# Kernel optimization log

Hardware: AMD Instinct MI355X
Metric: run time of the kernel (lower is better)

## Reference

```python
import jax, jax.numpy as jnp
import numpy as np

N_NODES = 50000

def _sage_conv(x, src, dst, W_l, b_l, W_r):
    # mean-aggregate neighbor features: messages x[src] summed into dst
    msgs = x[src]                                   # [E, d]
    agg = jax.ops.segment_sum(msgs, dst, num_segments=N_NODES)  # [N, d]
    ones = jnp.ones((src.shape[0],), dtype=x.dtype)
    cnt = jax.ops.segment_sum(ones, dst, num_segments=N_NODES)  # [N]
    agg = agg / jnp.maximum(cnt, 1.0)[:, None]
    return agg @ W_l + b_l + x @ W_r


def setup_inputs() -> dict:
    key = jax.random.key(0)
    ks = jax.random.split(key, 8)
    d_in, hid, out = 64, 128, 64
    x = jax.random.normal(ks[0], (N_NODES, d_in), dtype=jnp.float32)
    edge_index = jax.random.randint(ks[1], (2, 1600000), 0, N_NODES, dtype=jnp.int64)
    def w(k, a, b):
        return jax.random.normal(k, (a, b), dtype=jnp.float32) / np.sqrt(a)
    return {
        "x": x,
        "edge_index": edge_index,
        "W_l1": w(ks[2], d_in, hid), "b_l1": jnp.zeros((hid,), jnp.float32),
        "W_r1": w(ks[3], d_in, hid),
        "W_l2": w(ks[4], hid, hid), "b_l2": jnp.zeros((hid,), jnp.float32),
        "W_r2": w(ks[5], hid, hid),
        "W_out": w(ks[6], hid, out), "b_out": jnp.zeros((out,), jnp.float32),
    }


def reference(x, edge_index, W_l1, b_l1, W_r1, W_l2, b_l2, W_r2, W_out, b_out):
    src, dst = edge_index[0], edge_index[1]
    h = jax.nn.relu(_sage_conv(x, src, dst, W_l1, b_l1, W_r1))
    h = jax.nn.relu(_sage_conv(h, src, dst, W_l2, b_l2, W_r2))
    return h @ W_out + b_out
```

## Files before the change

### kernel.cpp

```cpp
#include <hip/hip_runtime.h>


typedef unsigned short ushort_t;
typedef unsigned int uint_t;
typedef unsigned char uchar_t;
typedef __attribute__((ext_vector_type(8))) short short8;
typedef __attribute__((ext_vector_type(8))) ushort_t ushort8;
typedef __attribute__((ext_vector_type(4))) float f32x4;

#define BKT_SHIFT 7
#define BKT_NODES 128
#define BKT_CAP   5120
#define EPB       4096
#define QSCALE    32.0f
#define QINV      0.03125f

__device__ inline ushort_t bf16_rne(float v) {
    uint_t u = __float_as_uint(v);
    u += 0x7fffu + ((u >> 16) & 1u);
    return (ushort_t)(u >> 16);
}
__device__ inline float bf16_to_f(ushort_t h) {
    return __uint_as_float((uint_t)h << 16);
}


struct WPack {
    const float* srcp[5];
    ushort_t* dstp[5];
    int K[5], N[5], beg[5], end[5];
};

__global__ __launch_bounds__(1024)
void k_work(const int* __restrict__ src, const int* __restrict__ dst,
            uint_t* __restrict__ pairs, int* __restrict__ bcnt, int E, int nbk,
            int bbl, const float* __restrict__ x, ushort_t* __restrict__ xh,
            ushort_t* __restrict__ xl, int NS, WPack wp, int total) {
    int tid = threadIdx.x;
    if (blockIdx.x >= bbl) {
        int t = (blockIdx.x - bbl) * 1024 + tid;
        if (t < NS) {
            float v = x[t];
            ushort_t h = bf16_rne(v);
            xh[t] = h;
            xl[t] = bf16_rne(v - bf16_to_f(h));
            return;
        }
        t -= NS;
        if (t >= total) return;
#pragma unroll
        for (int m = 0; m < 5; ++m) {
            if (t >= wp.beg[m] && t < wp.end[m]) {
                int i = t - wp.beg[m];
                int K = wp.K[m], N = wp.N[m];
                int k = i / N, nn = i % N;
                int NT = N >> 4;
                int kt = k >> 5, bq = (k >> 3) & 3, j = k & 7;
                int nt = nn >> 4, lane = (bq << 4) | (nn & 15);
                int base = (((kt * NT + nt) << 6) + lane) * 8 + j;
                int halfsz = (K >> 5) * NT * 512;
                float v = wp.srcp[m][i];
                ushort_t h = bf16_rne(v);
                wp.dstp[m][base] = h;
                wp.dstp[m][halfsz + base] = bf16_rne(v - bf16_to_f(h));
            }
        }
        return;
    }

    __shared__ int h[4][512];
    int sub = tid & 3;
    for (int i = tid; i < 4 * 512; i += 1024) ((int*)h)[i] = 0;
    __syncthreads();

    int e = blockIdx.x * EPB + tid * 4;
    bool full = (e + 4 <= E);
    int4 d4 = {0, 0, 0, 0}, s4 = {0, 0, 0, 0};
    if (full) {
        d4 = *(const int4*)(dst + e);
        s4 = *(const int4*)(src + e);
        atomicAdd(&h[sub][d4.x >> BKT_SHIFT], 1);
        atomicAdd(&h[sub][d4.y >> BKT_SHIFT], 1);
        atomicAdd(&h[sub][d4.z >> BKT_SHIFT], 1);
        atomicAdd(&h[sub][d4.w >> BKT_SHIFT], 1);
    } else {
        for (int t = e; t < E && t < e + 4; ++t)
            atomicAdd(&h[sub][dst[t] >> BKT_SHIFT], 1);
    }
    __syncthreads();
    for (int i = tid; i < nbk; i += 1024) {
        int c0 = h[0][i], c1 = h[1][i], c2 = h[2][i], c3 = h[3][i];
        int c = c0 + c1 + c2 + c3;
        int bs = c ? atomicAdd(&bcnt[i], c) : 0;
        h[0][i] = bs; h[1][i] = bs + c0; h[2][i] = bs + c0 + c1;
        h[3][i] = bs + c0 + c1 + c2;
    }
    __syncthreads();
    if (full) {
        int dd[4] = {d4.x, d4.y, d4.z, d4.w};
        int ss[4] = {s4.x, s4.y, s4.z, s4.w};
#pragma unroll
        for (int t = 0; t < 4; ++t) {
            int b = dd[t] >> BKT_SHIFT;
            int r = atomicAdd(&h[sub][b], 1);
            pairs[(size_t)b * BKT_CAP + r] =
                (uint_t)(ss[t] & 0xFFFF) | ((uint_t)(dd[t] & (BKT_NODES - 1)) << 16);
        }
    } else {
        for (int t = e; t < E && t < e + 4; ++t) {
            int d = dst[t];
            int b = d >> BKT_SHIFT;
            int r = atomicAdd(&h[sub][b], 1);
            pairs[(size_t)b * BKT_CAP + r] =
                (uint_t)(src[t] & 0xFFFF) | ((uint_t)(d & (BKT_NODES - 1)) << 16);
        }
    }
}


__global__ __launch_bounds__(1024) void k_csr(const uint_t* __restrict__ pairs,
                                              const int* __restrict__ bcnt,
                                              int* __restrict__ off,
                                              ushort_t* __restrict__ col, int n) {
    __shared__ int hist[BKT_NODES];
    __shared__ int s[BKT_NODES];
    __shared__ int cur[BKT_NODES];
    __shared__ int bofs_s;
    int b = blockIdx.x, tid = threadIdx.x;
    if (tid < 64) {
        int p = 0;
        for (int i = tid; i < b; i += 64) p += bcnt[i];
#pragma unroll
        for (int m = 1; m < 64; m <<= 1) p += __shfl_xor(p, m);
        if (tid == 0) bofs_s = p;
    }
    if (tid < BKT_NODES) hist[tid] = 0;
    __syncthreads();
    int bofs = bofs_s;
    int cnt = bcnt[b];
    const uint_t* p = pairs + (size_t)b * BKT_CAP;
    for (int i = tid; i < cnt; i += 1024) atomicAdd(&hist[(p[i] >> 16) & 127], 1);
    __syncthreads();
    int v = (tid < BKT_NODES) ? hist[tid] : 0;
    if (tid < BKT_NODES) s[tid] = v;
    __syncthreads();
    for (int ofs = 1; ofs < BKT_NODES; ofs <<= 1) {
        int t = (tid >= ofs && tid < BKT_NODES) ? s[tid - ofs] : 0;
        __syncthreads();
        if (tid < BKT_NODES) s[tid] += t;
        __syncthreads();
    }
    if (tid < BKT_NODES) {
        int excl = bofs + s[tid] - v;
        int node = b * BKT_NODES + tid;
        if (node <= n) off[node] = excl;
        cur[tid] = excl;
    }
    __syncthreads();
    for (int i = tid; i < cnt; i += 1024) {
        uint_t pk = p[i];
        int pos = atomicAdd(&cur[(pk >> 16) & 127], 1);
        col[pos] = (ushort_t)(pk & 0xFFFF);
    }
}


__device__ inline void accum2(float2 (&a)[4], uint4 q) {
    const uint_t* u = (const uint_t*)&q;
#pragma unroll
    for (int i = 0; i < 4; ++i) {
        a[i].x += __uint_as_float(u[i] << 16);
        a[i].y += __uint_as_float(u[i] & 0xffff0000u);
    }
}
__device__ inline void accum2m(float2 (&a)[4], uint4 q, float m) {
    const uint_t* u = (const uint_t*)&q;
#pragma unroll
    for (int i = 0; i < 4; ++i) {
        a[i].x = fmaf(m, __uint_as_float(u[i] << 16), a[i].x);
        a[i].y = fmaf(m, __uint_as_float(u[i] & 0xffff0000u), a[i].y);
    }
}

template <int DIN>
__device__ inline void agg_node(const ushort_t* __restrict__ fbase,
                                const ushort_t* __restrict__ col,
                                int s0, int s1, int sub, float2 (&a2)[4]) {
    constexpr int LPR = DIN / 8, EPI = 64 / LPR;
    constexpr int DEEP = (DIN == 128) ? 8 : 4;
#pragma unroll
    for (int j = 0; j < 4; ++j) a2[j] = (float2){0.f, 0.f};
    int e = s0;
    for (; e + DEEP * EPI <= s1; e += DEEP * EPI) {
        int c[DEEP];
        uint4 q[DEEP];
#pragma unroll
        for (int j = 0; j < DEEP; ++j) c[j] = col[e + j * EPI + sub];
#pragma unroll
        for (int j = 0; j < DEEP; ++j) q[j] = *(const uint4*)(fbase + (size_t)c[j] * DIN);
#pragma unroll
        for (int j = 0; j < DEEP; ++j) accum2(a2, q[j]);
    }
    for (; e < s1; e += 4 * EPI) {
        int last = s1 - 1;
        int i0 = e + sub, i1 = i0 + EPI, i2 = i1 + EPI, i3 = i2 + EPI;
        float m0 = (i0 < s1) ? 1.f : 0.f;
        float m1 = (i1 < s1) ? 1.f : 0.f;
        float m2 = (i2 < s1) ? 1.f : 0.f;
        float m3 = (i3 < s1) ? 1.f : 0.f;
        int c0 = col[min(i0, last)];
        int c1 = col[min(i1, last)];
        int c2 = col[min(i2, last)];
        int c3 = col[min(i3, last)];
        uint4 q0 = *(const uint4*)(fbase + (size_t)c0 * DIN);
        uint4 q1 = *(const uint4*)(fbase + (size_t)c1 * DIN);
        uint4 q2 = *(const uint4*)(fbase + (size_t)c2 * DIN);
        uint4 q3 = *(const uint4*)(fbase + (size_t)c3 * DIN);
        accum2m(a2, q0, m0); accum2m(a2, q1, m1);
        accum2m(a2, q2, m2); accum2m(a2, q3, m3);
    }
}

__global__ __launch_bounds__(256)
void k_agg_u8(const uchar_t* __restrict__ fq, const int* __restrict__ off,
              const ushort_t* __restrict__ col,
              ushort_t* __restrict__ ah, ushort_t* __restrict__ al, int n) {
    constexpr int EPI = 8;
    int wave = (int)((blockIdx.x * (unsigned)blockDim.x + threadIdx.x) >> 6);
    int lane = threadIdx.x & 63;
    if (wave >= n) return;
    int li = lane & 7;
    int sub = lane >> 3;
    int s0 = off[wave], s1 = off[wave + 1];
    const uchar_t* fbase = fq + li * 16;

    uint_t ae[4] = {0, 0, 0, 0}, ao[4] = {0, 0, 0, 0};
    int e = s0;
    for (; e + 4 * EPI <= s1; e += 4 * EPI) {
        int c[4];
        uint4 q[4];
#pragma unroll
        for (int j = 0; j < 4; ++j) c[j] = col[e + j * EPI + sub];
#pragma unroll
        for (int j = 0; j < 4; ++j) q[j] = *(const uint4*)(fbase + (size_t)c[j] * 128);
#pragma unroll
        for (int j = 0; j < 4; ++j) {
            const uint_t* u = (const uint_t*)&q[j];
#pragma unroll
            for (int i = 0; i < 4; ++i) {
                ae[i] += u[i] & 0x00FF00FFu;
                ao[i] += (u[i] >> 8) & 0x00FF00FFu;
            }
        }
    }
    if (e < s1) {
        int last = s1 - 1;
        int idx[4];
        uint_t msk[4];
        int c[4];
        uint4 q[4];
#pragma unroll
        for (int j = 0; j < 4; ++j) {
            idx[j] = e + j * EPI + sub;
            msk[j] = (idx[j] < s1) ? 0xFFFFFFFFu : 0u;
            c[j] = col[min(idx[j], last)];
        }
#pragma unroll
        for (int j = 0; j < 4; ++j) q[j] = *(const uint4*)(fbase + (size_t)c[j] * 128);
#pragma unroll
        for (int j = 0; j < 4; ++j) {
            const uint_t* u = (const uint_t*)&q[j];
#pragma unroll
            for (int i = 0; i < 4; ++i) {
                uint_t um = u[i] & msk[j];
                ae[i] += um & 0x00FF00FFu;
                ao[i] += (um >> 8) & 0x00FF00FFu;
            }
        }
    }
#pragma unroll
    for (int m = 8; m < 64; m <<= 1) {
#pragma unroll
        for (int i = 0; i < 4; ++i) {
            ae[i] += __shfl_xor(ae[i], m);
            ao[i] += __shfl_xor(ao[i], m);
        }
    }
    if (sub == 0) {
        float inv = QINV / fmaxf((float)(s1 - s0), 1.f);
        ushort_t vh[16], vl[16];
#pragma unroll
        for (int i = 0; i < 4; ++i) {
            uint_t f[4] = {ae[i] & 0xFFFFu, ao[i] & 0xFFFFu,
                           ae[i] >> 16, ao[i] >> 16};
#pragma unroll
            for (int b = 0; b < 4; ++b) {
                float mval = (float)f[b] * inv;
                ushort_t h = bf16_rne(mval);
                vh[i * 4 + b] = h;
                vl[i * 4 + b] = bf16_rne(mval - bf16_to_f(h));
            }
        }
        size_t o = (size_t)wave * 128 + li * 16;
        *(ushort8*)(ah + o) = *(ushort8*)&vh[0];
        *(ushort8*)(ah + o + 8) = *(ushort8*)&vh[8];
        *(ushort8*)(al + o) = *(ushort8*)&vl[0];
        *(ushort8*)(al + o + 8) = *(ushort8*)&vl[8];
    }
}

__device__ inline f32x4 mfma3(f32x4 acc, short8 ah, short8 al, short8 bh, short8 bl) {
    acc = __builtin_amdgcn_mfma_f32_16x16x32_bf16(ah, bh, acc, 0, 0, 0);
    acc = __builtin_amdgcn_mfma_f32_16x16x32_bf16(al, bh, acc, 0, 0, 0);
    acc = __builtin_amdgcn_mfma_f32_16x16x32_bf16(ah, bl, acc, 0, 0, 0);
    return acc;
}

template <int DIN, int DOUT, int M2>
__device__ inline void mfma_pass(const ushort_t* __restrict__ Fh,
                                 const ushort_t* __restrict__ Fl,
                                 const ushort_t* __restrict__ Wp,
                                 f32x4 (&acc)[M2][DOUT / 16],
                                 int base, int n, int lane) {
    constexpr int KT = DIN / 32, NT = DOUT / 16;
    int col = lane & 15, quad = lane >> 4;
    short8 fh[M2][KT], fl[M2][KT];
#pragma unroll
    for (int c = 0; c < M2; ++c) {
        int row = base + c * 16 + col;
        if (row >= n) row = n - 1;
        size_t roff = (size_t)row * DIN + quad * 8;
#pragma unroll
        for (int kt = 0; kt < KT; ++kt) {
            fh[c][kt] = *(const short8*)(Fh + roff + kt * 32);
            fl[c][kt] = *(const short8*)(Fl + roff + kt * 32);
        }
    }
#pragma unroll
    for (int nt = 0; nt < NT; ++nt) {
#pragma unroll
        for (int kt = 0; kt < KT; ++kt) {
            const ushort_t* p = Wp + ((size_t)((kt * NT + nt) << 6) + lane) * 8;
            short8 bh = *(const short8*)p;
            short8 bl = *(const short8*)(p + (size_t)KT * NT * 512);
#pragma unroll
            for (int c = 0; c < M2; ++c)
                acc[c][nt] = mfma3(acc[c][nt], fh[c][kt], fl[c][kt], bh, bl);
        }
    }
}


__global__ __launch_bounds__(512)
void k_layer1(const ushort_t* __restrict__ xh, const ushort_t* __restrict__ xl,
              const int* __restrict__ off, const ushort_t* __restrict__ col,
              const ushort_t* __restrict__ Wlp, const ushort_t* __restrict__ Wrp,
              const float* __restrict__ bias, ushort_t* __restrict__ Oh,
              ushort_t* __restrict__ Ol, uchar_t* __restrict__ Oq, int n) {
    constexpr int LPR = 8;
    __shared__ ushort_t Ahs[32][72];
    __shared__ ushort_t Als[32][72];
    int tid = threadIdx.x, waveid = tid >> 6, lane = tid & 63;
    int base = blockIdx.x * 32;
    int li = lane & (LPR - 1);
    int sub = lane / LPR;

    for (int q = 0; q < 4; ++q) {
        int node = base + waveid * 4 + q;
        int nd = node < n ? node : n - 1;
        int s0 = off[nd], s1 = off[nd + 1];
        float2 a2[4];
        agg_node<64>(xh + li * 8, col, s0, s1, sub, a2);
#pragma unroll
        for (int m = LPR; m < 64; m <<= 1) {
#pragma unroll
            for (int j = 0; j < 4; ++j) {
                a2[j].x += __shfl_xor(a2[j].x, m);
                a2[j].y += __shfl_xor(a2[j].y, m);
            }
        }
        if (sub == 0) {
            float inv = 1.f / fmaxf((float)(s1 - s0), 1.f);
            ushort8 vh, vl;
#pragma unroll
            for (int j = 0; j < 4; ++j) {
                float mx = a2[j].x * inv, my = a2[j].y * inv;
                ushort_t hx = bf16_rne(mx), hy = bf16_rne(my);
                vh[2 * j] = hx;     vl[2 * j] = bf16_rne(mx - bf16_to_f(hx));
                vh[2 * j + 1] = hy; vl[2 * j + 1] = bf16_rne(my - bf16_to_f(hy));
            }
            *(ushort8*)&Ahs[waveid * 4 + q][li * 8] = vh;
            *(ushort8*)&Als[waveid * 4 + q][li * 8] = vl;
        }
    }
    __syncthreads();

    int rowt = waveid >> 2, c0 = waveid & 3;
    int colq = lane & 15, quad = lane >> 4;
    int arow = rowt * 16 + colq;
    short8 fah[2], fal[2], fxh[2], fxl[2];
#pragma unroll
    for (int kt = 0; kt < 2; ++kt) {
        fah[kt] = *(const short8*)&Ahs[arow][kt * 32 + quad * 8];
        fal[kt] = *(const short8*)&Als[arow][kt * 32 + quad * 8];
    }
    int grow = base + arow; if (grow >= n) grow = n - 1;
#pragma unroll
    for (int kt = 0; kt < 2; ++kt) {
        fxh[kt] = *(const short8*)(xh + (size_t)grow * 64 + kt * 32 + quad * 8);
        fxl[kt] = *(const short8*)(xl + (size_t)grow * 64 + kt * 32 + quad * 8);
    }
#pragma unroll
    for (int t = 0; t < 2; ++t) {
        int nt = c0 + t * 4;
        float bv = bias[nt * 16 + colq];
        f32x4 acc = (f32x4){bv, bv, bv, bv};
#pragma unroll
        for (int kt = 0; kt < 2; ++kt) {
            const ushort_t* pL = Wlp + ((size_t)((kt * 8 + nt) << 6) + lane) * 8;
            acc = mfma3(acc, fah[kt], fal[kt],
                        *(const short8*)pL, *(const short8*)(pL + 8192));
            const ushort_t* pR = Wrp + ((size_t)((kt * 8 + nt) << 6) + lane) * 8;
            acc = mfma3(acc, fxh[kt], fxl[kt],
                        *(const short8*)pR, *(const short8*)(pR + 8192));
        }
        int rowb = base + rowt * 16 + quad * 4;
        int cix = nt * 16 + colq;
#pragma unroll
        for (int r = 0; r < 4; ++r) {
            int row = rowb + r;
            if (row < n) {
                float v = fmaxf(acc[r], 0.f);
                ushort_t h = bf16_rne(v);
                Oh[(size_t)row * 128 + cix] = h;
                Ol[(size_t)row * 128 + cix] = bf16_rne(v - bf16_to_f(h));
                int qv = (int)(v * QSCALE + 0.5f);
                Oq[(size_t)row * 128 + cix] = (uchar_t)(qv > 255 ? 255 : qv);
            }
        }
    }
}


#define LROW 136
__global__ __launch_bounds__(256)
void k_dense23(const ushort_t* __restrict__ Ah, const ushort_t* __restrict__ Al,
               const ushort_t* __restrict__ Xh, const ushort_t* __restrict__ Xl,
               const ushort_t* __restrict__ Wlp, const ushort_t* __restrict__ Wrp,
               const float* __restrict__ b2, const ushort_t* __restrict__ Wop,
               const float* __restrict__ bo, float* __restrict__ out, int n) {
    constexpr int DIN = 128, DOUT = 128, NT = DOUT / 16;
    __shared__ ushort_t lds[4][2][16 * LROW];
    int waveid = threadIdx.x >> 6;
    int lane = threadIdx.x & 63;
    int wave = (blockIdx.x * blockDim.x + threadIdx.x) >> 6;
    int nw = (n + 15) / 16;
    if (wave >= nw) wave = nw - 1;
    int base = wave * 16;
    int col = lane & 15, quad = lane >> 4;

    f32x4 acc[1][NT];
#pragma unroll
    for (int nt = 0; nt < NT; ++nt) {
        float bv = b2[nt * 16 + col];
        acc[0][nt] = (f32x4){bv, bv, bv, bv};
    }
    mfma_pass<DIN, DOUT, 1>(Ah, Al, Wlp, acc, base, n, lane);
    mfma_pass<DIN, DOUT, 1>(Xh, Xl, Wrp, acc, base, n, lane);

    ushort_t* Lh = &lds[waveid][0][0];
    ushort_t* Ll = &lds[waveid][1][0];
#pragma unroll
    for (int nt = 0; nt < NT; ++nt) {
        int cix = nt * 16 + col;
#pragma unroll
        for (int r = 0; r < 4; ++r) {
            int row = quad * 4 + r;
            float v = fmaxf(acc[0][nt][r], 0.f);
            ushort_t h = bf16_rne(v);
            Lh[row * LROW + cix] = h;
            Ll[row * LROW + cix] = bf16_rne(v - bf16_to_f(h));
        }
    }
    __syncthreads();

    constexpr int KT2 = 4, NT2 = 4;
    short8 ah[KT2], al[KT2];
    int arow = lane & 15;
#pragma unroll
    for (int kt = 0; kt < KT2; ++kt) {
        ah[kt] = *(const short8*)(Lh + arow * LROW + kt * 32 + quad * 8);
        al[kt] = *(const short8*)(Ll + arow * LROW + kt * 32 + quad * 8);
    }
    f32x4 acc2[NT2];
#pragma unroll
    for (int nt = 0; nt < NT2; ++nt) {
        float bv = bo[nt * 16 + col];
        acc2[nt] = (f32x4){bv, bv, bv, bv};
    }
#pragma unroll
    for (int nt = 0; nt < NT2; ++nt) {
#pragma unroll
        for (int kt = 0; kt < KT2; ++kt) {
            const ushort_t* p = Wop + ((size_t)((kt * 4 + nt) << 6) + lane) * 8;
            acc2[nt] = mfma3(acc2[nt], ah[kt], al[kt],
                             *(const short8*)p, *(const short8*)(p + 8192));
        }
    }
    int rowb = base + quad * 4;
#pragma unroll
    for (int nt = 0; nt < NT2; ++nt) {
        int cix = nt * 16 + col;
#pragma unroll
        for (int r = 0; r < 4; ++r) {
            int row = rowb + r;
            if (row < n) out[(size_t)row * 64 + cix] = acc2[nt][r];
        }
    }
}


static inline size_t align256(size_t x) { return (x + 255) & ~(size_t)255; }

extern "C" void kernel_launch(void* const* d_in, const int* in_sizes, int n_in,
                              void* d_out, int out_size, void* d_ws, size_t ws_size,
                              hipStream_t stream) {
    const float* x   = (const float*)d_in[0];
    const int*   ei  = (const int*)d_in[1];
    const float* Wl1 = (const float*)d_in[2];
    const float* bl1 = (const float*)d_in[3];
    const float* Wr1 = (const float*)d_in[4];
    const float* Wl2 = (const float*)d_in[5];
    const float* bl2 = (const float*)d_in[6];
    const float* Wr2 = (const float*)d_in[7];
    const float* Wo  = (const float*)d_in[8];
    const float* bo  = (const float*)d_in[9];

    const int N = in_sizes[0] / 64;
    const int E = in_sizes[1] / 2;
    const int* src = ei;
    const int* dst = ei + E;
    const int nbk = (N + BKT_NODES - 1) >> BKT_SHIFT;

    char* ws = (char*)d_ws;
    int* off = (int*)ws;            ws += align256((size_t)(N + 1) * 4);
    int* bcnt = (int*)ws;           ws += align256((size_t)nbk * 4);
    uint_t* pairs = (uint_t*)ws;    ws += align256((size_t)nbk * BKT_CAP * 4);
    ushort_t* col = (ushort_t*)ws;  ws += align256((size_t)E * 2);
    ushort_t* xh  = (ushort_t*)ws;  ws += align256((size_t)N * 64 * 2);
    ushort_t* xl  = (ushort_t*)ws;  ws += align256((size_t)N * 64 * 2);
    ushort_t* h1h = (ushort_t*)ws;  ws += align256((size_t)N * 128 * 2);
    ushort_t* h1l = (ushort_t*)ws;  ws += align256((size_t)N * 128 * 2);
    uchar_t*  h1q = (uchar_t*)ws;   ws += align256((size_t)N * 128);
    ushort_t* a2h = (ushort_t*)ws;  ws += align256((size_t)N * 128 * 2);
    ushort_t* a2l = (ushort_t*)ws;  ws += align256((size_t)N * 128 * 2);
    ushort_t* Wl1p = (ushort_t*)ws; ws += align256((size_t)2 * 64 * 128 * 2);
    ushort_t* Wr1p = (ushort_t*)ws; ws += align256((size_t)2 * 64 * 128 * 2);
    ushort_t* Wl2p = (ushort_t*)ws; ws += align256((size_t)2 * 128 * 128 * 2);
    ushort_t* Wr2p = (ushort_t*)ws; ws += align256((size_t)2 * 128 * 128 * 2);
    ushort_t* Wop  = (ushort_t*)ws; ws += align256((size_t)2 * 128 * 64 * 2);

    WPack wp;
    wp.srcp[0] = Wl1; wp.dstp[0] = Wl1p; wp.K[0] = 64;  wp.N[0] = 128;
    wp.srcp[1] = Wr1; wp.dstp[1] = Wr1p; wp.K[1] = 64;  wp.N[1] = 128;
    wp.srcp[2] = Wl2; wp.dstp[2] = Wl2p; wp.K[2] = 128; wp.N[2] = 128;
    wp.srcp[3] = Wr2; wp.dstp[3] = Wr2p; wp.K[3] = 128; wp.N[3] = 128;
    wp.srcp[4] = Wo;  wp.dstp[4] = Wop;  wp.K[4] = 128; wp.N[4] = 64;
    int acc_el = 0;
    for (int m = 0; m < 5; ++m) {
        wp.beg[m] = acc_el; acc_el += wp.K[m] * wp.N[m]; wp.end[m] = acc_el;
    }
    int NS = N * 64;

    hipMemsetAsync(bcnt, 0, (size_t)nbk * 4, stream);
    int bbl = (E + EPB - 1) / EPB;
    int pbl = (NS + acc_el + 1023) / 1024;
    k_work<<<bbl + pbl, 1024, 0, stream>>>(src, dst, pairs, bcnt, E, nbk, bbl,
                                           x, xh, xl, NS, wp, acc_el);

    k_csr<<<nbk, 1024, 0, stream>>>(pairs, bcnt, off, col, N);

    k_layer1<<<(N + 31) / 32, 512, 0, stream>>>(xh, xl, off, col, Wl1p, Wr1p,
                                                bl1, h1h, h1l, h1q, N);

    int aggbl = (N * 64 + 255) / 256;
    k_agg_u8<<<aggbl, 256, 0, stream>>>(h1q, off, col, a2h, a2l, N);

    int dbl2 = ((N + 15) / 16 + 3) / 4;
    k_dense23<<<dbl2, 256, 0, stream>>>(a2h, a2l, h1h, h1l, Wl2p, Wr2p, bl2,
                                        Wop, bo, (float*)d_out, N);
}
```

Measured before the change: 231.6 us.

## Quantize layer-1 gather to uint8 and fuse layer-2 aggregation with dense stages

```diff
diff --git a/kernel.cpp b/kernel.cpp
--- a/kernel.cpp
+++ b/kernel.cpp
@@ -14,6 +14,7 @@
 #define EPB       4096
 #define QSCALE    32.0f
 #define QINV      0.03125f
+#define XQSCALE   16.0f
 
 __device__ inline ushort_t bf16_rne(float v) {
     uint_t u = __float_as_uint(v);
@@ -35,7 +36,8 @@
 void k_work(const int* __restrict__ src, const int* __restrict__ dst,
             uint_t* __restrict__ pairs, int* __restrict__ bcnt, int E, int nbk,
             int bbl, const float* __restrict__ x, ushort_t* __restrict__ xh,
-            ushort_t* __restrict__ xl, int NS, WPack wp, int total) {
+            ushort_t* __restrict__ xl, uchar_t* __restrict__ xq,
+            int NS, WPack wp, int total) {
     int tid = threadIdx.x;
     if (blockIdx.x >= bbl) {
         int t = (blockIdx.x - bbl) * 1024 + tid;
@@ -44,6 +46,9 @@
             ushort_t h = bf16_rne(v);
             xh[t] = h;
             xl[t] = bf16_rne(v - bf16_to_f(h));
+            int qv = (int)(v * XQSCALE + 128.5f);
+            qv = qv < 0 ? 0 : (qv > 255 ? 255 : qv);
+            xq[t] = (uchar_t)qv;
             return;
         }
         t -= NS;
@@ -164,77 +169,14 @@
     }
 }
 
-
-__device__ inline void accum2(float2 (&a)[4], uint4 q) {
-    const uint_t* u = (const uint_t*)&q;
-#pragma unroll
-    for (int i = 0; i < 4; ++i) {
-        a[i].x += __uint_as_float(u[i] << 16);
-        a[i].y += __uint_as_float(u[i] & 0xffff0000u);
-    }
-}
-__device__ inline void accum2m(float2 (&a)[4], uint4 q, float m) {
-    const uint_t* u = (const uint_t*)&q;
-#pragma unroll
-    for (int i = 0; i < 4; ++i) {
-        a[i].x = fmaf(m, __uint_as_float(u[i] << 16), a[i].x);
-        a[i].y = fmaf(m, __uint_as_float(u[i] & 0xffff0000u), a[i].y);
-    }
-}
-
-template <int DIN>
-__device__ inline void agg_node(const ushort_t* __restrict__ fbase,
-                                const ushort_t* __restrict__ col,
-                                int s0, int s1, int sub, float2 (&a2)[4]) {
-    constexpr int LPR = DIN / 8, EPI = 64 / LPR;
-    constexpr int DEEP = (DIN == 128) ? 8 : 4;
-#pragma unroll
-    for (int j = 0; j < 4; ++j) a2[j] = (float2){0.f, 0.f};
-    int e = s0;
-    for (; e + DEEP * EPI <= s1; e += DEEP * EPI) {
-        int c[DEEP];
-        uint4 q[DEEP];
-#pragma unroll
-        for (int j = 0; j < DEEP; ++j) c[j] = col[e + j * EPI + sub];
-#pragma unroll
-        for (int j = 0; j < DEEP; ++j) q[j] = *(const uint4*)(fbase + (size_t)c[j] * DIN);
-#pragma unroll
-        for (int j = 0; j < DEEP; ++j) accum2(a2, q[j]);
-    }
-    for (; e < s1; e += 4 * EPI) {
-        int last = s1 - 1;
-        int i0 = e + sub, i1 = i0 + EPI, i2 = i1 + EPI, i3 = i2 + EPI;
-        float m0 = (i0 < s1) ? 1.f : 0.f;
-        float m1 = (i1 < s1) ? 1.f : 0.f;
-        float m2 = (i2 < s1) ? 1.f : 0.f;
-        float m3 = (i3 < s1) ? 1.f : 0.f;
-        int c0 = col[min(i0, last)];
-        int c1 = col[min(i1, last)];
-        int c2 = col[min(i2, last)];
-        int c3 = col[min(i3, last)];
-        uint4 q0 = *(const uint4*)(fbase + (size_t)c0 * DIN);
-        uint4 q1 = *(const uint4*)(fbase + (size_t)c1 * DIN);
-        uint4 q2 = *(const uint4*)(fbase + (size_t)c2 * DIN);
-        uint4 q3 = *(const uint4*)(fbase + (size_t)c3 * DIN);
-        accum2m(a2, q0, m0); accum2m(a2, q1, m1);
-        accum2m(a2, q2, m2); accum2m(a2, q3, m3);
-    }
-}
-
-__global__ __launch_bounds__(256)
-void k_agg_u8(const uchar_t* __restrict__ fq, const int* __restrict__ off,
-              const ushort_t* __restrict__ col,
-              ushort_t* __restrict__ ah, ushort_t* __restrict__ al, int n) {
-    constexpr int EPI = 8;
-    int wave = (int)((blockIdx.x * (unsigned)blockDim.x + threadIdx.x) >> 6);
-    int lane = threadIdx.x & 63;
-    if (wave >= n) return;
-    int li = lane & 7;
-    int sub = lane >> 3;
-    int s0 = off[wave], s1 = off[wave + 1];
-    const uchar_t* fbase = fq + li * 16;
-
-    uint_t ae[4] = {0, 0, 0, 0}, ao[4] = {0, 0, 0, 0};
+template <int ROWB>
+__device__ inline void gather_u8(const uchar_t* __restrict__ fbase,
+                                 const ushort_t* __restrict__ col,
+                                 int s0, int s1, int sub,
+                                 uint_t (&ae)[4], uint_t (&ao)[4]) {
+    constexpr int EPI = 1024 / ROWB;
+#pragma unroll
+    for (int i = 0; i < 4; ++i) { ae[i] = 0u; ao[i] = 0u; }
     int e = s0;
     for (; e + 4 * EPI <= s1; e += 4 * EPI) {
         int c[4];
@@ -242,7 +184,7 @@
 #pragma unroll
         for (int j = 0; j < 4; ++j) c[j] = col[e + j * EPI + sub];
 #pragma unroll
-        for (int j = 0; j < 4; ++j) q[j] = *(const uint4*)(fbase + (size_t)c[j] * 128);
+        for (int j = 0; j < 4; ++j) q[j] = *(const uint4*)(fbase + (size_t)c[j] * ROWB);
 #pragma unroll
         for (int j = 0; j < 4; ++j) {
             const uint_t* u = (const uint_t*)&q[j];
@@ -253,22 +195,21 @@
             }
         }
     }
-    if (e < s1) {
+    for (; e < s1; e += 2 * EPI) {
         int last = s1 - 1;
-        int idx[4];
-        uint_t msk[4];
-        int c[4];
-        uint4 q[4];
-#pragma unroll
-        for (int j = 0; j < 4; ++j) {
-            idx[j] = e + j * EPI + sub;
-            msk[j] = (idx[j] < s1) ? 0xFFFFFFFFu : 0u;
-            c[j] = col[min(idx[j], last)];
-        }
-#pragma unroll
-        for (int j = 0; j < 4; ++j) q[j] = *(const uint4*)(fbase + (size_t)c[j] * 128);
-#pragma unroll
-        for (int j = 0; j < 4; ++j) {
+        int c[2];
+        uint_t msk[2];
+        uint4 q[2];
+#pragma unroll
+        for (int j = 0; j < 2; ++j) {
+            int idx = e + j * EPI + sub;
+            msk[j] = (idx < s1) ? 0xFFFFFFFFu : 0u;
+            c[j] = col[min(idx, last)];
+        }
+#pragma unroll
+        for (int j = 0; j < 2; ++j) q[j] = *(const uint4*)(fbase + (size_t)c[j] * ROWB);
+#pragma unroll
+        for (int j = 0; j < 2; ++j) {
             const uint_t* u = (const uint_t*)&q[j];
 #pragma unroll
             for (int i = 0; i < 4; ++i) {
@@ -277,35 +218,6 @@
                 ao[i] += (um >> 8) & 0x00FF00FFu;
             }
         }
-    }
-#pragma unroll
-    for (int m = 8; m < 64; m <<= 1) {
-#pragma unroll
-        for (int i = 0; i < 4; ++i) {
-            ae[i] += __shfl_xor(ae[i], m);
-            ao[i] += __shfl_xor(ao[i], m);
-        }
-    }
-    if (sub == 0) {
-        float inv = QINV / fmaxf((float)(s1 - s0), 1.f);
-        ushort_t vh[16], vl[16];
-#pragma unroll
-        for (int i = 0; i < 4; ++i) {
-            uint_t f[4] = {ae[i] & 0xFFFFu, ao[i] & 0xFFFFu,
-                           ae[i] >> 16, ao[i] >> 16};
-#pragma unroll
-            for (int b = 0; b < 4; ++b) {
-                float mval = (float)f[b] * inv;
-                ushort_t h = bf16_rne(mval);
-                vh[i * 4 + b] = h;
-                vl[i * 4 + b] = bf16_rne(mval - bf16_to_f(h));
-            }
-        }
-        size_t o = (size_t)wave * 128 + li * 16;
-        *(ushort8*)(ah + o) = *(ushort8*)&vh[0];
-        *(ushort8*)(ah + o + 8) = *(ushort8*)&vh[8];
-        *(ushort8*)(al + o) = *(ushort8*)&vl[0];
-        *(ushort8*)(al + o + 8) = *(ushort8*)&vl[8];
     }
 }
 
@@ -316,81 +228,58 @@
     return acc;
 }
 
-template <int DIN, int DOUT, int M2>
-__device__ inline void mfma_pass(const ushort_t* __restrict__ Fh,
-                                 const ushort_t* __restrict__ Fl,
-                                 const ushort_t* __restrict__ Wp,
-                                 f32x4 (&acc)[M2][DOUT / 16],
-                                 int base, int n, int lane) {
-    constexpr int KT = DIN / 32, NT = DOUT / 16;
-    int col = lane & 15, quad = lane >> 4;
-    short8 fh[M2][KT], fl[M2][KT];
-#pragma unroll
-    for (int c = 0; c < M2; ++c) {
-        int row = base + c * 16 + col;
-        if (row >= n) row = n - 1;
-        size_t roff = (size_t)row * DIN + quad * 8;
-#pragma unroll
-        for (int kt = 0; kt < KT; ++kt) {
-            fh[c][kt] = *(const short8*)(Fh + roff + kt * 32);
-            fl[c][kt] = *(const short8*)(Fl + roff + kt * 32);
-        }
-    }
-#pragma unroll
-    for (int nt = 0; nt < NT; ++nt) {
-#pragma unroll
-        for (int kt = 0; kt < KT; ++kt) {
-            const ushort_t* p = Wp + ((size_t)((kt * NT + nt) << 6) + lane) * 8;
-            short8 bh = *(const short8*)p;
-            short8 bl = *(const short8*)(p + (size_t)KT * NT * 512);
-#pragma unroll
-            for (int c = 0; c < M2; ++c)
-                acc[c][nt] = mfma3(acc[c][nt], fh[c][kt], fl[c][kt], bh, bl);
-        }
-    }
-}
-
 
 __global__ __launch_bounds__(512)
-void k_layer1(const ushort_t* __restrict__ xh, const ushort_t* __restrict__ xl,
+void k_layer1(const uchar_t* __restrict__ xq, const ushort_t* __restrict__ xh,
+              const ushort_t* __restrict__ xl,
               const int* __restrict__ off, const ushort_t* __restrict__ col,
               const ushort_t* __restrict__ Wlp, const ushort_t* __restrict__ Wrp,
               const float* __restrict__ bias, ushort_t* __restrict__ Oh,
-              ushort_t* __restrict__ Ol, uchar_t* __restrict__ Oq, int n) {
-    constexpr int LPR = 8;
+              uchar_t* __restrict__ Oq, int n) {
     __shared__ ushort_t Ahs[32][72];
     __shared__ ushort_t Als[32][72];
     int tid = threadIdx.x, waveid = tid >> 6, lane = tid & 63;
     int base = blockIdx.x * 32;
-    int li = lane & (LPR - 1);
-    int sub = lane / LPR;
+    int li = lane & 3;
+    int sub = lane >> 2;
+    const uchar_t* fbase = xq + li * 16;
 
     for (int q = 0; q < 4; ++q) {
         int node = base + waveid * 4 + q;
         int nd = node < n ? node : n - 1;
         int s0 = off[nd], s1 = off[nd + 1];
-        float2 a2[4];
-        agg_node<64>(xh + li * 8, col, s0, s1, sub, a2);
-#pragma unroll
-        for (int m = LPR; m < 64; m <<= 1) {
-#pragma unroll
-            for (int j = 0; j < 4; ++j) {
-                a2[j].x += __shfl_xor(a2[j].x, m);
-                a2[j].y += __shfl_xor(a2[j].y, m);
+        uint_t ae[4], ao[4];
+        gather_u8<64>(fbase, col, s0, s1, sub, ae, ao);
+#pragma unroll
+        for (int m = 4; m < 64; m <<= 1) {
+#pragma unroll
+            for (int i = 0; i < 4; ++i) {
+                ae[i] += __shfl_xor(ae[i], m);
+                ao[i] += __shfl_xor(ao[i], m);
             }
         }
         if (sub == 0) {
-            float inv = 1.f / fmaxf((float)(s1 - s0), 1.f);
-            ushort8 vh, vl;
-#pragma unroll
-            for (int j = 0; j < 4; ++j) {
-                float mx = a2[j].x * inv, my = a2[j].y * inv;
-                ushort_t hx = bf16_rne(mx), hy = bf16_rne(my);
-                vh[2 * j] = hx;     vl[2 * j] = bf16_rne(mx - bf16_to_f(hx));
-                vh[2 * j + 1] = hy; vl[2 * j + 1] = bf16_rne(my - bf16_to_f(hy));
-            }
-            *(ushort8*)&Ahs[waveid * 4 + q][li * 8] = vh;
-            *(ushort8*)&Als[waveid * 4 + q][li * 8] = vl;
+            int deg = s1 - s0;
+            float inv = 1.f / (XQSCALE * fmaxf((float)deg, 1.f));
+            float c8 = deg > 0 ? 8.f : 0.f;
+            ushort_t vh[16], vl[16];
+#pragma unroll
+            for (int i = 0; i < 4; ++i) {
+                uint_t f[4] = {ae[i] & 0xFFFFu, ao[i] & 0xFFFFu,
+                               ae[i] >> 16, ao[i] >> 16};
+#pragma unroll
+                for (int b = 0; b < 4; ++b) {
+                    float mval = (float)f[b] * inv - c8;
+                    ushort_t h = bf16_rne(mval);
+                    vh[i * 4 + b] = h;
+                    vl[i * 4 + b] = bf16_rne(mval - bf16_to_f(h));
+                }
+            }
+            int r = waveid * 4 + q;
+            *(ushort8*)&Ahs[r][li * 16] = *(ushort8*)&vh[0];
+            *(ushort8*)&Ahs[r][li * 16 + 8] = *(ushort8*)&vh[8];
+            *(ushort8*)&Als[r][li * 16] = *(ushort8*)&vl[0];
+            *(ushort8*)&Als[r][li * 16 + 8] = *(ushort8*)&vl[8];
         }
     }
     __syncthreads();
@@ -431,9 +320,7 @@
             int row = rowb + r;
             if (row < n) {
                 float v = fmaxf(acc[r], 0.f);
-                ushort_t h = bf16_rne(v);
-                Oh[(size_t)row * 128 + cix] = h;
-                Ol[(size_t)row * 128 + cix] = bf16_rne(v - bf16_to_f(h));
+                Oh[(size_t)row * 128 + cix] = bf16_rne(v);
                 int qv = (int)(v * QSCALE + 0.5f);
                 Oq[(size_t)row * 128 + cix] = (uchar_t)(qv > 255 ? 255 : qv);
             }
@@ -442,80 +329,115 @@
 }
 
 
-#define LROW 136
+#define L2R 136
 __global__ __launch_bounds__(256)
-void k_dense23(const ushort_t* __restrict__ Ah, const ushort_t* __restrict__ Al,
-               const ushort_t* __restrict__ Xh, const ushort_t* __restrict__ Xl,
-               const ushort_t* __restrict__ Wlp, const ushort_t* __restrict__ Wrp,
-               const float* __restrict__ b2, const ushort_t* __restrict__ Wop,
-               const float* __restrict__ bo, float* __restrict__ out, int n) {
-    constexpr int DIN = 128, DOUT = 128, NT = DOUT / 16;
-    __shared__ ushort_t lds[4][2][16 * LROW];
-    int waveid = threadIdx.x >> 6;
-    int lane = threadIdx.x & 63;
-    int wave = (blockIdx.x * blockDim.x + threadIdx.x) >> 6;
-    int nw = (n + 15) / 16;
-    if (wave >= nw) wave = nw - 1;
-    int base = wave * 16;
-    int col = lane & 15, quad = lane >> 4;
-
-    f32x4 acc[1][NT];
-#pragma unroll
-    for (int nt = 0; nt < NT; ++nt) {
-        float bv = b2[nt * 16 + col];
-        acc[0][nt] = (f32x4){bv, bv, bv, bv};
-    }
-    mfma_pass<DIN, DOUT, 1>(Ah, Al, Wlp, acc, base, n, lane);
-    mfma_pass<DIN, DOUT, 1>(Xh, Xl, Wrp, acc, base, n, lane);
-
-    ushort_t* Lh = &lds[waveid][0][0];
-    ushort_t* Ll = &lds[waveid][1][0];
-#pragma unroll
-    for (int nt = 0; nt < NT; ++nt) {
-        int cix = nt * 16 + col;
+void k_layer2(const uchar_t* __restrict__ h1q, const int* __restrict__ off,
+              const ushort_t* __restrict__ col, const ushort_t* __restrict__ h1h,
+              const ushort_t* __restrict__ Wlp, const ushort_t* __restrict__ Wrp,
+              const float* __restrict__ b2, const ushort_t* __restrict__ Wop,
+              const float* __restrict__ bo, float* __restrict__ out, int n) {
+    __shared__ ushort_t Ah[16][L2R], Al[16][L2R];
+    __shared__ ushort_t Hh[16][L2R], Hl[16][L2R];
+    int tid = threadIdx.x, waveid = tid >> 6, lane = tid & 63;
+    int base = blockIdx.x * 16;
+    int li = lane & 7;
+    int sub = lane >> 3;
+    const uchar_t* fbase = h1q + li * 16;
+
+    for (int q = 0; q < 4; ++q) {
+        int node = base + waveid * 4 + q;
+        int nd = node < n ? node : n - 1;
+        int s0 = off[nd], s1 = off[nd + 1];
+        uint_t ae[4], ao[4];
+        gather_u8<128>(fbase, col, s0, s1, sub, ae, ao);
+#pragma unroll
+        for (int m = 8; m < 64; m <<= 1) {
+#pragma unroll
+            for (int i = 0; i < 4; ++i) {
+                ae[i] += __shfl_xor(ae[i], m);
+                ao[i] += __shfl_xor(ao[i], m);
+            }
+        }
+        if (sub == 0) {
+            float inv = QINV / fmaxf((float)(s1 - s0), 1.f);
+            ushort_t vh[16], vl[16];
+#pragma unroll
+            for (int i = 0; i < 4; ++i) {
+                uint_t f[4] = {ae[i] & 0xFFFFu, ao[i] & 0xFFFFu,
+                               ae[i] >> 16, ao[i] >> 16};
+#pragma unroll
+                for (int b = 0; b < 4; ++b) {
+                    float mval = (float)f[b] * inv;
+                    ushort_t h = bf16_rne(mval);
+                    vh[i * 4 + b] = h;
+                    vl[i * 4 + b] = bf16_rne(mval - bf16_to_f(h));
+                }
+            }
+            int r = waveid * 4 + q;
+            *(ushort8*)&Ah[r][li * 16] = *(ushort8*)&vh[0];
+            *(ushort8*)&Ah[r][li * 16 + 8] = *(ushort8*)&vh[8];
+            *(ushort8*)&Al[r][li * 16] = *(ushort8*)&vl[0];
+            *(ushort8*)&Al[r][li * 16 + 8] = *(ushort8*)&vl[8];
+        }
+    }
+    __syncthreads();
+
+    int colx = lane & 15, quad = lane >> 4;
+    int arow = colx;
+    int grow = base + arow; if (grow >= n) grow = n - 1;
+    short8 gah[4], gal[4], sh[4];
+#pragma unroll
+    for (int kt = 0; kt < 4; ++kt) {
+        gah[kt] = *(const short8*)&Ah[arow][kt * 32 + quad * 8];
+        gal[kt] = *(const short8*)&Al[arow][kt * 32 + quad * 8];
+        sh[kt]  = *(const short8*)(h1h + (size_t)grow * 128 + kt * 32 + quad * 8);
+    }
+#pragma unroll
+    for (int t = 0; t < 2; ++t) {
+        int nt = waveid + t * 4;
+        float bv = b2[nt * 16 + colx];
+        f32x4 acc = (f32x4){bv, bv, bv, bv};
+#pragma unroll
+        for (int kt = 0; kt < 4; ++kt) {
+            const ushort_t* pL = Wlp + ((size_t)((kt * 8 + nt) << 6) + lane) * 8;
+            acc = mfma3(acc, gah[kt], gal[kt],
+                        *(const short8*)pL, *(const short8*)(pL + 16384));
+            const ushort_t* pR = Wrp + ((size_t)((kt * 8 + nt) << 6) + lane) * 8;
+            short8 bh = *(const short8*)pR;
+            short8 bl = *(const short8*)(pR + 16384);
+            acc = __builtin_amdgcn_mfma_f32_16x16x32_bf16(sh[kt], bh, acc, 0, 0, 0);
+            acc = __builtin_amdgcn_mfma_f32_16x16x32_bf16(sh[kt], bl, acc, 0, 0, 0);
+        }
 #pragma unroll
         for (int r = 0; r < 4; ++r) {
             int row = quad * 4 + r;
-            float v = fmaxf(acc[0][nt][r], 0.f);
+            float v = fmaxf(acc[r], 0.f);
             ushort_t h = bf16_rne(v);
-            Lh[row * LROW + cix] = h;
-            Ll[row * LROW + cix] = bf16_rne(v - bf16_to_f(h));
-        }
-    }
-    __syncthreads();
-
-    constexpr int KT2 = 4, NT2 = 4;
-    short8 ah[KT2], al[KT2];
-    int arow = lane & 15;
-#pragma unroll
-    for (int kt = 0; kt < KT2; ++kt) {
-        ah[kt] = *(const short8*)(Lh + arow * LROW + kt * 32 + quad * 8);
-        al[kt] = *(const short8*)(Ll + arow * LROW + kt * 32 + quad * 8);
-    }
-    f32x4 acc2[NT2];
-#pragma unroll
-    for (int nt = 0; nt < NT2; ++nt) {
-        float bv = bo[nt * 16 + col];
-        acc2[nt] = (f32x4){bv, bv, bv, bv};
-    }
-#pragma unroll
-    for (int nt = 0; nt < NT2; ++nt) {
-#pragma unroll
-        for (int kt = 0; kt < KT2; ++kt) {
-            const ushort_t* p = Wop + ((size_t)((kt * 4 + nt) << 6) + lane) * 8;
-            acc2[nt] = mfma3(acc2[nt], ah[kt], al[kt],
-                             *(const short8*)p, *(const short8*)(p + 8192));
-        }
-    }
-    int rowb = base + quad * 4;
-#pragma unroll
-    for (int nt = 0; nt < NT2; ++nt) {
-        int cix = nt * 16 + col;
-#pragma unroll
-        for (int r = 0; r < 4; ++r) {
-            int row = rowb + r;
-            if (row < n) out[(size_t)row * 64 + cix] = acc2[nt][r];
-        }
+            Hh[row][nt * 16 + colx] = h;
+            Hl[row][nt * 16 + colx] = bf16_rne(v - bf16_to_f(h));
+        }
+    }
+    __syncthreads();
+
+    short8 hh[4], hl[4];
+#pragma unroll
+    for (int kt = 0; kt < 4; ++kt) {
+        hh[kt] = *(const short8*)&Hh[arow][kt * 32 + quad * 8];
+        hl[kt] = *(const short8*)&Hl[arow][kt * 32 + quad * 8];
+    }
+    int nt2 = waveid;
+    float bv = bo[nt2 * 16 + colx];
+    f32x4 acc2 = (f32x4){bv, bv, bv, bv};
+#pragma unroll
+    for (int kt = 0; kt < 4; ++kt) {
+        const ushort_t* p = Wop + ((size_t)((kt * 4 + nt2) << 6) + lane) * 8;
+        acc2 = mfma3(acc2, hh[kt], hl[kt],
+                     *(const short8*)p, *(const short8*)(p + 8192));
+    }
+#pragma unroll
+    for (int r = 0; r < 4; ++r) {
+        int row = base + quad * 4 + r;
+        if (row < n) out[(size_t)row * 64 + nt2 * 16 + colx] = acc2[r];
     }
 }
 
@@ -549,11 +471,9 @@
     ushort_t* col = (ushort_t*)ws;  ws += align256((size_t)E * 2);
     ushort_t* xh  = (ushort_t*)ws;  ws += align256((size_t)N * 64 * 2);
     ushort_t* xl  = (ushort_t*)ws;  ws += align256((size_t)N * 64 * 2);
+    uchar_t*  xq  = (uchar_t*)ws;   ws += align256((size_t)N * 64);
     ushort_t* h1h = (ushort_t*)ws;  ws += align256((size_t)N * 128 * 2);
-    ushort_t* h1l = (ushort_t*)ws;  ws += align256((size_t)N * 128 * 2);
     uchar_t*  h1q = (uchar_t*)ws;   ws += align256((size_t)N * 128);
-    ushort_t* a2h = (ushort_t*)ws;  ws += align256((size_t)N * 128 * 2);
-    ushort_t* a2l = (ushort_t*)ws;  ws += align256((size_t)N * 128 * 2);
     ushort_t* Wl1p = (ushort_t*)ws; ws += align256((size_t)2 * 64 * 128 * 2);
     ushort_t* Wr1p = (ushort_t*)ws; ws += align256((size_t)2 * 64 * 128 * 2);
     ushort_t* Wl2p = (ushort_t*)ws; ws += align256((size_t)2 * 128 * 128 * 2);
@@ -576,17 +496,13 @@
     int bbl = (E + EPB - 1) / EPB;
     int pbl = (NS + acc_el + 1023) / 1024;
     k_work<<<bbl + pbl, 1024, 0, stream>>>(src, dst, pairs, bcnt, E, nbk, bbl,
-                                           x, xh, xl, NS, wp, acc_el);
+                                           x, xh, xl, xq, NS, wp, acc_el);
 
     k_csr<<<nbk, 1024, 0, stream>>>(pairs, bcnt, off, col, N);
 
-    k_layer1<<<(N + 31) / 32, 512, 0, stream>>>(xh, xl, off, col, Wl1p, Wr1p,
-                                                bl1, h1h, h1l, h1q, N);
-
-    int aggbl = (N * 64 + 255) / 256;
-    k_agg_u8<<<aggbl, 256, 0, stream>>>(h1q, off, col, a2h, a2l, N);
-
-    int dbl2 = ((N + 15) / 16 + 3) / 4;
-    k_dense23<<<dbl2, 256, 0, stream>>>(a2h, a2l, h1h, h1l, Wl2p, Wr2p, bl2,
-                                        Wop, bo, (float*)d_out, N);
-}
+    k_layer1<<<(N + 31) / 32, 512, 0, stream>>>(xq, xh, xl, off, col, Wl1p,
+                                                Wr1p, bl1, h1h, h1q, N);
+
+    k_layer2<<<(N + 15) / 16, 256, 0, stream>>>(h1q, off, col, h1h, Wl2p, Wr2p,
+                                                bl2, Wop, bo, (float*)d_out, N);
+}
```

Result: faster. 216.8 us (-6.4%).
